# Kernel tuning notes

Hardware: AMD Instinct MI355X
Metric: run time of the kernel (lower is better)

Reference implementation:

```python
import jax, jax.numpy as jnp
import numpy as np

T, B, D_IN = 128, 256, 600   # timesteps, batch, encoded input dim
N_RIMS, K_ACT = 6, 4          # rims per layer, active rims (top-k)
D_HID = 600 // N_RIMS         # hidden dim per RIM = 100
D_K, D_V = 64, 400            # input-attention key/value proj dims (in_d_v = cell input dim)


def setup_inputs() -> dict:
    key = jax.random.key(0)
    ks = jax.random.split(key, 8)
    g = lambda k, shape, s: (jax.random.normal(k, shape, jnp.float32) * s)
    return {
        "x": jax.random.normal(ks[0], (T, B, D_IN), jnp.float32),
        # input attention: per-RIM query proj, shared key/value proj over encoded input
        "Wq": g(ks[1], (N_RIMS, D_HID, D_K), 0.05),
        "Wk": g(ks[2], (D_IN, D_K), 0.05),
        "Wv": g(ks[3], (D_IN, D_V), 0.05),
        # block-diagonal (per-RIM) GRU params
        "W_ih": g(ks[4], (N_RIMS, D_V, 3 * D_HID), 0.05),
        "W_hh": g(ks[5], (N_RIMS, D_HID, 3 * D_HID), 0.05),
        "b_ih": jnp.zeros((N_RIMS, 3 * D_HID), jnp.float32),
        "b_hh": jnp.zeros((N_RIMS, 3 * D_HID), jnp.float32),
    }


def reference(x, Wq, Wk, Wv, W_ih, W_hh, b_ih, b_hh):
    scale = 1.0 / jnp.sqrt(jnp.float32(D_K))

    def step(h, xt):
        # --- input attention over [real input, null row] (num_modules_read_input = 2) ---
        kx = xt @ Wk                                   # [B, D_K] key for real input (null key = 0)
        vx = xt @ Wv                                   # [B, D_V] value for real input (null value = 0)
        q = jnp.einsum('bnh,nhk->bnk', h, Wq)          # [B, N, D_K] per-RIM queries
        s_in = jnp.einsum('bnk,bk->bn', q, kx) * scale # score vs real input; null score = 0
        probs = jax.nn.softmax(jnp.stack([s_in, jnp.zeros_like(s_in)], axis=-1), axis=-1)
        p_in = probs[..., 0]                           # [B, N] attention on real input
        attn_out = p_in[..., None] * vx[:, None, :]    # [B, N, D_V] (null value is zero)
        # --- active-RIM mask: top-k rims attending most to the real input ---
        _, idx = jax.lax.top_k(p_in, K_ACT)            # [B, K]
        mask = jnp.zeros_like(p_in).at[jnp.arange(B)[:, None], idx].set(1.0)[..., None]  # [B, N, 1]
        # --- block-diagonal GRU cell (blockified params: independent per RIM) ---
        gi = jnp.einsum('bnd,ndk->bnk', attn_out, W_ih) + b_ih
        gh = jnp.einsum('bnh,nhk->bnk', h, W_hh) + b_hh
        i_r, i_z, i_n = jnp.split(gi, 3, axis=-1)
        h_r, h_z, h_n = jnp.split(gh, 3, axis=-1)
        r = jax.nn.sigmoid(i_r + h_r)
        z = jax.nn.sigmoid(i_z + h_z)
        n = jnp.tanh(i_n + r * h_n)
        h_new = (1.0 - z) * n + z * h
        # inactive rims keep their old state; output is mask * hidden
        h_next = mask * h_new + (1.0 - mask) * h
        return h_next, mask * h_new                    # [B, N, D_HID]

    h0 = jnp.zeros((B, N_RIMS, D_HID), x.dtype)
    _, out = jax.lax.scan(step, h0, x)                 # out: [T, B, N_RIMS, D_HID]
    return out
```

## Files before the change

kernel.cpp:

```cpp
#include <hip/hip_runtime.h>
#include <cstddef>

#define TSTEPS 128
#define BATCH  256
#define DIN    600
#define NR     6
#define KACT   4
#define DH     100
#define DK     64
#define DV     400
#define G3     300
#define LD1    512
#define LDG    1920
#define KB     8

__global__ __launch_bounds__(256) void build_w1(const float* __restrict__ Wk,
                                                const float* __restrict__ Wv,
                                                float* __restrict__ W1) {
  int idx = blockIdx.x * 256 + threadIdx.x;
  if (idx >= DIN * LD1) return;
  int d = idx >> 9, c = idx & (LD1 - 1);
  float v = 0.f;
  if (c < DK)            v = Wk[d * DK + c];
  else if (c < DK + DV)  v = Wv[d * DV + (c - DK)];
  W1[idx] = v;
}

__global__ __launch_bounds__(256) void build_wt(const float* __restrict__ Wih,
                                                float* __restrict__ WT) {
  int idx = blockIdx.x * 256 + threadIdx.x;
  if (idx >= DV * LDG) return;
  int v = idx / LDG, c = idx - v * LDG;
  float w = 0.f;
  if (c < NR * G3) { int n = c / G3, j = c - n * G3; w = Wih[(n * DV + v) * G3 + j]; }
  WT[idx] = w;
}

__global__ __launch_bounds__(256) void sgemm_k(const float* __restrict__ A, int lda,
                                               const float* __restrict__ B, int ldb,
                                               float* __restrict__ C, int ldc, int K) {
  __shared__ float As[2][KB][132];
  __shared__ float Bs[2][KB][192];
  const int tid = threadIdx.x;
  const int tx = tid & 15, ty = tid >> 4;
  const size_t m0 = (size_t)blockIdx.y * 128, n0 = (size_t)blockIdx.x * 128;
  const int arow = tid >> 1, akq = (tid & 1) * 4;
  const int brow = tid >> 5, bcol = (tid & 31) * 4;
  const int bphys = bcol + ((bcol >> 3) << 2);
  const float* Ap = A + (m0 + arow) * (size_t)lda + akq;
  const float* Bp = B + (size_t)brow * ldb + n0 + bcol;

  float acc[8][8];
#pragma unroll
  for (int i = 0; i < 8; ++i)
#pragma unroll
    for (int j = 0; j < 8; ++j) acc[i][j] = 0.f;

  const int NT = K / KB;
  float4 av = *(const float4*)(Ap);
  float4 bv = *(const float4*)(Bp);
  As[0][akq + 0][arow] = av.x;
  As[0][akq + 1][arow] = av.y;
  As[0][akq + 2][arow] = av.z;
  As[0][akq + 3][arow] = av.w;
  *(float4*)&Bs[0][brow][bphys] = bv;
  __syncthreads();

  int cur = 0;
  for (int it = 0; it < NT; ++it) {
    if (it + 1 < NT) {
      av = *(const float4*)(Ap + (it + 1) * KB);
      bv = *(const float4*)(Bp + (size_t)(it + 1) * KB * ldb);
    }
#pragma unroll
    for (int k = 0; k < KB; ++k) {
      float a[8], b[8];
      *(float4*)&a[0] = *(const float4*)&As[cur][k][ty * 8];
      *(float4*)&a[4] = *(const float4*)&As[cur][k][ty * 8 + 4];
      *(float4*)&b[0] = *(const float4*)&Bs[cur][k][tx * 12];
      *(float4*)&b[4] = *(const float4*)&Bs[cur][k][tx * 12 + 4];
#pragma unroll
      for (int i = 0; i < 8; ++i)
#pragma unroll
        for (int j = 0; j < 8; ++j) acc[i][j] += a[i] * b[j];
    }
    if (it + 1 < NT) {
      const int nxt = cur ^ 1;
      As[nxt][akq + 0][arow] = av.x;
      As[nxt][akq + 1][arow] = av.y;
      As[nxt][akq + 2][arow] = av.z;
      As[nxt][akq + 3][arow] = av.w;
      *(float4*)&Bs[nxt][brow][bphys] = bv;
      __syncthreads();
      cur = nxt;
    }
  }

  float* Cp = C + (m0 + (size_t)ty * 8) * ldc + n0 + tx * 8;
#pragma unroll
  for (int i = 0; i < 8; ++i) {
    float4 v0 = make_float4(acc[i][0], acc[i][1], acc[i][2], acc[i][3]);
    float4 v1 = make_float4(acc[i][4], acc[i][5], acc[i][6], acc[i][7]);
    *(float4*)(Cp + (size_t)i * ldc)     = v0;
    *(float4*)(Cp + (size_t)i * ldc + 4) = v1;
  }
}

__global__ __launch_bounds__(512) void rim_scan(
    const float* __restrict__ PRE1, const float* __restrict__ GX,
    const float* __restrict__ Wq,   const float* __restrict__ Whh,
    const float* __restrict__ bih,  const float* __restrict__ bhh,
    float* __restrict__ out, float* __restrict__ hstate,
    unsigned long long* __restrict__ pbuf,
    int t0, int tc, int first) {
  __shared__ __align__(16) float wbuf[G3 * DH];
  __shared__ __align__(16) float wqbuf[DK * DH];
  __shared__ __align__(16) float hbuf[8 * DH];
  __shared__ float pl[8][NR];

  const int tid = threadIdx.x;
  const int g = blockIdx.x & 31;
  const int n = blockIdx.x >> 5;

  {
    const float* wsrc = Whh + (size_t)n * (DH * G3);
    for (int i = tid; i < DH * G3; i += 512) {
      int hh = i / G3, c = i - hh * G3;
      wbuf[c * DH + hh] = wsrc[i];
    }
    const float* qsrc = Wq + (size_t)n * (DH * DK);
    for (int i = tid; i < DH * DK; i += 512) {
      int hh = i >> 6, k = i & 63;
      wqbuf[k * DH + hh] = qsrc[i];
    }
    if (first) {
      for (int i = tid; i < 8 * DH; i += 512) hbuf[i] = 0.f;
    } else {
      for (int i = tid; i < 8 * DH; i += 512) {
        int b = i / DH, hh = i - b * DH;
        hbuf[b * DH + hh] = hstate[((size_t)(g * 8 + b) * NR + n) * DH + hh];
      }
    }
  }
  __syncthreads();

  const bool isQ = tid >= 256;
  const int ho = tid & 127;
  const bool act_t = (!isQ) && (ho < DH);
  const int half = (tid >> 7) & 1;
  const int bbase = half * 4;
  const int kq = tid & 63;
  const int bp2 = (tid >> 6) & 3;

  float bi0 = 0.f, bi1 = 0.f, bi2 = 0.f, bh0 = 0.f, bh1 = 0.f, bh2 = 0.f;
  if (act_t) {
    const float* bi = bih + (size_t)n * G3 + ho;
    const float* bh = bhh + (size_t)n * G3 + ho;
    bi0 = bi[0]; bi1 = bi[DH]; bi2 = bi[2 * DH];
    bh0 = bh[0]; bh1 = bh[DH]; bh2 = bh[2 * DH];
  }

  const float4* wr = (const float4*)&wbuf[ho * DH];
  const float4* wz = (const float4*)&wbuf[(ho + 100) * DH];
  const float4* wn = (const float4*)&wbuf[(ho + 200) * DH];
  const float4* wq4 = (const float4*)&wqbuf[kq * DH];
  const float4* h40 = (const float4*)&hbuf[(bbase + 0) * DH];
  const float4* h41 = (const float4*)&hbuf[(bbase + 1) * DH];
  const float4* h42 = (const float4*)&hbuf[(bbase + 2) * DH];
  const float4* h43 = (const float4*)&hbuf[(bbase + 3) * DH];
  const float4* hqA = (const float4*)&hbuf[bp2 * DH];
  const float4* hqB = (const float4*)&hbuf[(bp2 + 4) * DH];

  for (int tl = 0; tl < tc; ++tl) {
    const int t = t0 + tl;
    const int par = t & 1;

    float gx[4][3];
    float acc[4][3];

    if (isQ) {
      float kx0 = PRE1[((size_t)tl * BATCH + g * 8 + bp2) * LD1 + kq];
      float kx1 = PRE1[((size_t)tl * BATCH + g * 8 + bp2 + 4) * LD1 + kq];
      float a0 = 0.f, a1 = 0.f;
#pragma unroll 5
      for (int q4 = 0; q4 < 25; ++q4) {
        float4 w = wq4[q4];
        float4 v0 = hqA[q4];
        float4 v1 = hqB[q4];
        a0 += v0.x * w.x; a0 += v0.y * w.y; a0 += v0.z * w.z; a0 += v0.w * w.w;
        a1 += v1.x * w.x; a1 += v1.y * w.y; a1 += v1.z * w.z; a1 += v1.w * w.w;
      }
      float s0 = a0 * kx0, s1 = a1 * kx1;
#pragma unroll
      for (int off = 1; off < 64; off <<= 1) {
        s0 += __shfl_xor(s0, off);
        s1 += __shfl_xor(s1, off);
      }
      if (kq == 0) {
        float sa = s0 * 0.125f;
        float ma = sa > 0.f ? sa : 0.f;
        float pa = expf(sa - ma) / (expf(sa - ma) + expf(-ma));
        float sb = s1 * 0.125f;
        float mb = sb > 0.f ? sb : 0.f;
        float pb = expf(sb - mb) / (expf(sb - mb) + expf(-mb));
        unsigned long long tag = ((unsigned long long)(unsigned)(t + 1)) << 32;
        __hip_atomic_store(&pbuf[(((size_t)par * 32 + g) * NR + n) * 8 + bp2],
                           tag | __float_as_uint(pa),
                           __ATOMIC_RELAXED, __HIP_MEMORY_SCOPE_AGENT);
        __hip_atomic_store(&pbuf[(((size_t)par * 32 + g) * NR + n) * 8 + bp2 + 4],
                           tag | __float_as_uint(pb),
                           __ATOMIC_RELAXED, __HIP_MEMORY_SCOPE_AGENT);
      }
    } else if (act_t) {
#pragma unroll
      for (int b = 0; b < 4; ++b) {
        const float* gr = GX + ((size_t)tl * BATCH + g * 8 + bbase + b) * LDG + n * G3;
        gx[b][0] = gr[ho]; gx[b][1] = gr[ho + DH]; gx[b][2] = gr[ho + 2 * DH];
      }
#pragma unroll
      for (int b = 0; b < 4; ++b) { acc[b][0] = 0.f; acc[b][1] = 0.f; acc[b][2] = 0.f; }
#pragma unroll 5
      for (int q4 = 0; q4 < 25; ++q4) {
        float4 w0 = wr[q4], w1 = wz[q4], w2 = wn[q4];
        float4 v0 = h40[q4], v1 = h41[q4], v2 = h42[q4], v3 = h43[q4];
        acc[0][0] += v0.x*w0.x; acc[0][0] += v0.y*w0.y; acc[0][0] += v0.z*w0.z; acc[0][0] += v0.w*w0.w;
        acc[0][1] += v0.x*w1.x; acc[0][1] += v0.y*w1.y; acc[0][1] += v0.z*w1.z; acc[0][1] += v0.w*w1.w;
        acc[0][2] += v0.x*w2.x; acc[0][2] += v0.y*w2.y; acc[0][2] += v0.z*w2.z; acc[0][2] += v0.w*w2.w;
        acc[1][0] += v1.x*w0.x; acc[1][0] += v1.y*w0.y; acc[1][0] += v1.z*w0.z; acc[1][0] += v1.w*w0.w;
        acc[1][1] += v1.x*w1.x; acc[1][1] += v1.y*w1.y; acc[1][1] += v1.z*w1.z; acc[1][1] += v1.w*w1.w;
        acc[1][2] += v1.x*w2.x; acc[1][2] += v1.y*w2.y; acc[1][2] += v1.z*w2.z; acc[1][2] += v1.w*w2.w;
        acc[2][0] += v2.x*w0.x; acc[2][0] += v2.y*w0.y; acc[2][0] += v2.z*w0.z; acc[2][0] += v2.w*w0.w;
        acc[2][1] += v2.x*w1.x; acc[2][1] += v2.y*w1.y; acc[2][1] += v2.z*w1.z; acc[2][1] += v2.w*w1.w;
        acc[2][2] += v2.x*w2.x; acc[2][2] += v2.y*w2.y; acc[2][2] += v2.z*w2.z; acc[2][2] += v2.w*w2.w;
        acc[3][0] += v3.x*w0.x; acc[3][0] += v3.y*w0.y; acc[3][0] += v3.z*w0.z; acc[3][0] += v3.w*w0.w;
        acc[3][1] += v3.x*w1.x; acc[3][1] += v3.y*w1.y; acc[3][1] += v3.z*w1.z; acc[3][1] += v3.w*w1.w;
        acc[3][2] += v3.x*w2.x; acc[3][2] += v3.y*w2.y; acc[3][2] += v3.z*w2.z; acc[3][2] += v3.w*w2.w;
      }
    }

    if (tid < 48) {
      int b = tid & 7, r = tid >> 3;
      const unsigned want = (unsigned)(t + 1);
      unsigned long long v;
      for (;;) {
        v = __hip_atomic_load(&pbuf[(((size_t)par * 32 + g) * NR + r) * 8 + b],
                              __ATOMIC_RELAXED, __HIP_MEMORY_SCOPE_AGENT);
        if ((unsigned)(v >> 32) == want) break;
        __builtin_amdgcn_s_sleep(1);
      }
      pl[b][r] = __uint_as_float((unsigned)v);
    }
    __syncthreads();

    if (act_t) {
#pragma unroll
      for (int b = 0; b < 4; ++b) {
        const int bb = bbase + b;
        float p = pl[bb][n];
        int c = 0;
#pragma unroll
        for (int r = 0; r < NR; ++r) {
          float q = pl[bb][r];
          if (q > p || (q == p && r < n)) ++c;
        }
        float m = (c < KACT) ? 1.f : 0.f;
        float grv = acc[b][0] + bh0;
        float gzv = acc[b][1] + bh1;
        float gnv = acc[b][2] + bh2;
        float ir  = p * gx[b][0] + bi0;
        float iz  = p * gx[b][1] + bi1;
        float inn = p * gx[b][2] + bi2;
        float rr = 1.f / (1.f + expf(-(ir + grv)));
        float zz = 1.f / (1.f + expf(-(iz + gzv)));
        float nn = tanhf(inn + rr * gnv);
        float hprev = hbuf[bb * DH + ho];
        float hnew = (1.f - zz) * nn + zz * hprev;
        out[(((size_t)t * BATCH + g * 8 + bb) * NR + n) * DH + ho] = m * hnew;
        hbuf[bb * DH + ho] = (m > 0.f) ? hnew : hprev;
      }
    }
    __syncthreads();
  }

  for (int i = tid; i < 8 * DH; i += 512) {
    int b = i / DH, hh = i - b * DH;
    hstate[((size_t)(g * 8 + b) * NR + n) * DH + hh] = hbuf[b * DH + hh];
  }
}

extern "C" void kernel_launch(void* const* d_in, const int* in_sizes, int n_in,
                              void* d_out, int out_size, void* d_ws, size_t ws_size,
                              hipStream_t stream) {
  const float* x   = (const float*)d_in[0];
  const float* Wq  = (const float*)d_in[1];
  const float* Wk  = (const float*)d_in[2];
  const float* Wv  = (const float*)d_in[3];
  const float* Wih = (const float*)d_in[4];
  const float* Whh = (const float*)d_in[5];
  const float* bih = (const float*)d_in[6];
  const float* bhh = (const float*)d_in[7];
  float* out = (float*)d_out;
  char* ws = (char*)d_ws;

  const size_t W1_BYTES   = (size_t)DIN * LD1 * 4;
  const size_t WT_BYTES   = (size_t)DV * LDG * 4;
  const size_t H_BYTES    = (size_t)BATCH * 600 * 4;
  const size_t PBUF_BYTES = 2 * 32 * NR * 8 * 8;
  const size_t FIXED = W1_BYTES + WT_BYTES + H_BYTES + PBUF_BYTES;
  const size_t PER_STEP = (size_t)BATCH * (LD1 + LDG) * 4;

  float* W1     = (float*)ws;
  float* WT     = (float*)(ws + W1_BYTES);
  float* hstate = (float*)(ws + W1_BYTES + WT_BYTES);
  unsigned long long* pbuf =
      (unsigned long long*)(ws + W1_BYTES + WT_BYTES + H_BYTES);

  long long avail = (long long)ws_size - (long long)FIXED;
  int TC = 1;
  if (avail > 0) {
    long long t = avail / (long long)PER_STEP;
    TC = (int)(t < 1 ? 1 : (t > TSTEPS ? TSTEPS : t));
  }
  float* PRE1 = (float*)(ws + FIXED);
  float* GXb  = (float*)(ws + FIXED + (size_t)TC * BATCH * LD1 * 4);

  build_w1<<<(DIN * LD1) / 256, 256, 0, stream>>>(Wk, Wv, W1);
  build_wt<<<(DV * LDG) / 256, 256, 0, stream>>>(Wih, WT);

  for (int t0 = 0; t0 < TSTEPS; ) {
    int tc = TSTEPS - t0 < TC ? TSTEPS - t0 : TC;
    dim3 g1(LD1 / 128, tc * 2);
    sgemm_k<<<g1, 256, 0, stream>>>(x + (size_t)t0 * BATCH * DIN, DIN, W1, LD1, PRE1, LD1, DIN);
    dim3 g2(LDG / 128, tc * 2);
    sgemm_k<<<g2, 256, 0, stream>>>(PRE1 + DK, LD1, WT, LDG, GXb, LDG, DV);
    rim_scan<<<32 * NR, 512, 0, stream>>>(PRE1, GXb, Wq, Whh, bih, bhh, out, hstate,
                                          pbuf, t0, tc, t0 == 0 ? 1 : 0);
    t0 += tc;
  }
}
```

Before: 1.905 ms.

## Repack W_hh into paired-column shared layout with two outputs per thread

Each GH thread now handles two adjacent hidden columns instead of one, which halves the active threads per half-batch from 100 to 50 lanes. W_hh is repacked in shared memory as float4 tiles interleaving two rows and two columns, so consecutive lanes read consecutive float4s with fewer bank conflicts. Loads of GX, stores to out and hbuf become float2 vectors. The aim is better LDS access efficiency and more register reuse of h values. The cost is fewer active lanes doing more serial work each, which may lengthen the critical path of every timestep.

```diff
diff --git a/kernel.cpp b/kernel.cpp
--- a/kernel.cpp
+++ b/kernel.cpp
@@ -113,7 +113,7 @@
     float* __restrict__ out, float* __restrict__ hstate,
     unsigned long long* __restrict__ pbuf,
     int t0, int tc, int first) {
-  __shared__ __align__(16) float wbuf[G3 * DH];
+  __shared__ __align__(16) float wpbuf[50 * 3 * 50 * 4];
   __shared__ __align__(16) float wqbuf[DK * DH];
   __shared__ __align__(16) float hbuf[8 * DH];
   __shared__ float pl[8][NR];
@@ -124,9 +124,18 @@
 
   {
     const float* wsrc = Whh + (size_t)n * (DH * G3);
-    for (int i = tid; i < DH * G3; i += 512) {
-      int hh = i / G3, c = i - hh * G3;
-      wbuf[c * DH + hh] = wsrc[i];
+    for (int i = tid; i < 50 * 3 * 50; i += 512) {
+      int ph = i / 150;
+      int r  = i - ph * 150;
+      int gg = r / 50;
+      int cp = r - gg * 50;
+      const float* base = wsrc + (2 * ph) * G3 + gg * 100 + 2 * cp;
+      float4 q;
+      q.x = base[0];
+      q.y = base[1];
+      q.z = base[G3];
+      q.w = base[G3 + 1];
+      *(float4*)&wpbuf[i * 4] = q;
     }
     const float* qsrc = Wq + (size_t)n * (DH * DK);
     for (int i = tid; i < DH * DK; i += 512) {
@@ -145,29 +154,33 @@
   __syncthreads();
 
   const bool isQ = tid >= 256;
-  const int ho = tid & 127;
-  const bool act_t = (!isQ) && (ho < DH);
-  const int half = (tid >> 7) & 1;
-  const int bbase = half * 4;
+  const int wv = tid >> 6, lane = tid & 63;
+  const bool ghA = (wv < 2) && (lane < 50);
+  const int bh = wv & 1;
+  const int cp = lane;
+  const int bbase = bh * 4;
   const int kq = tid & 63;
   const int bp2 = (tid >> 6) & 3;
 
-  float bi0 = 0.f, bi1 = 0.f, bi2 = 0.f, bh0 = 0.f, bh1 = 0.f, bh2 = 0.f;
-  if (act_t) {
-    const float* bi = bih + (size_t)n * G3 + ho;
-    const float* bh = bhh + (size_t)n * G3 + ho;
-    bi0 = bi[0]; bi1 = bi[DH]; bi2 = bi[2 * DH];
-    bh0 = bh[0]; bh1 = bh[DH]; bh2 = bh[2 * DH];
-  }
-
-  const float4* wr = (const float4*)&wbuf[ho * DH];
-  const float4* wz = (const float4*)&wbuf[(ho + 100) * DH];
-  const float4* wn = (const float4*)&wbuf[(ho + 200) * DH];
+  float bi_[3][2], bh_[3][2];
+  if (ghA) {
+#pragma unroll
+    for (int gg = 0; gg < 3; ++gg)
+#pragma unroll
+      for (int c = 0; c < 2; ++c) {
+        bi_[gg][c] = bih[(size_t)n * G3 + gg * 100 + 2 * cp + c];
+        bh_[gg][c] = bhh[(size_t)n * G3 + gg * 100 + 2 * cp + c];
+      }
+  }
+
+  const float4* wp = (const float4*)wpbuf;
   const float4* wq4 = (const float4*)&wqbuf[kq * DH];
-  const float4* h40 = (const float4*)&hbuf[(bbase + 0) * DH];
-  const float4* h41 = (const float4*)&hbuf[(bbase + 1) * DH];
-  const float4* h42 = (const float4*)&hbuf[(bbase + 2) * DH];
-  const float4* h43 = (const float4*)&hbuf[(bbase + 3) * DH];
+  const float4* hq4[4] = {
+    (const float4*)&hbuf[(bbase + 0) * DH],
+    (const float4*)&hbuf[(bbase + 1) * DH],
+    (const float4*)&hbuf[(bbase + 2) * DH],
+    (const float4*)&hbuf[(bbase + 3) * DH]
+  };
   const float4* hqA = (const float4*)&hbuf[bp2 * DH];
   const float4* hqB = (const float4*)&hbuf[(bp2 + 4) * DH];
 
@@ -175,8 +188,8 @@
     const int t = t0 + tl;
     const int par = t & 1;
 
-    float gx[4][3];
-    float acc[4][3];
+    float gx[4][3][2];
+    float acc[4][3][2];
 
     if (isQ) {
       float kx0 = PRE1[((size_t)tl * BATCH + g * 8 + bp2) * LD1 + kq];
@@ -211,30 +224,38 @@
                            tag | __float_as_uint(pb),
                            __ATOMIC_RELAXED, __HIP_MEMORY_SCOPE_AGENT);
       }
-    } else if (act_t) {
+    } else if (ghA) {
 #pragma unroll
       for (int b = 0; b < 4; ++b) {
         const float* gr = GX + ((size_t)tl * BATCH + g * 8 + bbase + b) * LDG + n * G3;
-        gx[b][0] = gr[ho]; gx[b][1] = gr[ho + DH]; gx[b][2] = gr[ho + 2 * DH];
-      }
-#pragma unroll
-      for (int b = 0; b < 4; ++b) { acc[b][0] = 0.f; acc[b][1] = 0.f; acc[b][2] = 0.f; }
+#pragma unroll
+        for (int gg = 0; gg < 3; ++gg) {
+          float2 v = *(const float2*)(gr + gg * 100 + 2 * cp);
+          gx[b][gg][0] = v.x; gx[b][gg][1] = v.y;
+        }
+      }
+#pragma unroll
+      for (int b = 0; b < 4; ++b)
+#pragma unroll
+        for (int gg = 0; gg < 3; ++gg) { acc[b][gg][0] = 0.f; acc[b][gg][1] = 0.f; }
 #pragma unroll 5
-      for (int q4 = 0; q4 < 25; ++q4) {
-        float4 w0 = wr[q4], w1 = wz[q4], w2 = wn[q4];
-        float4 v0 = h40[q4], v1 = h41[q4], v2 = h42[q4], v3 = h43[q4];
-        acc[0][0] += v0.x*w0.x; acc[0][0] += v0.y*w0.y; acc[0][0] += v0.z*w0.z; acc[0][0] += v0.w*w0.w;
-        acc[0][1] += v0.x*w1.x; acc[0][1] += v0.y*w1.y; acc[0][1] += v0.z*w1.z; acc[0][1] += v0.w*w1.w;
-        acc[0][2] += v0.x*w2.x; acc[0][2] += v0.y*w2.y; acc[0][2] += v0.z*w2.z; acc[0][2] += v0.w*w2.w;
-        acc[1][0] += v1.x*w0.x; acc[1][0] += v1.y*w0.y; acc[1][0] += v1.z*w0.z; acc[1][0] += v1.w*w0.w;
-        acc[1][1] += v1.x*w1.x; acc[1][1] += v1.y*w1.y; acc[1][1] += v1.z*w1.z; acc[1][1] += v1.w*w1.w;
-        acc[1][2] += v1.x*w2.x; acc[1][2] += v1.y*w2.y; acc[1][2] += v1.z*w2.z; acc[1][2] += v1.w*w2.w;
-        acc[2][0] += v2.x*w0.x; acc[2][0] += v2.y*w0.y; acc[2][0] += v2.z*w0.z; acc[2][0] += v2.w*w0.w;
-        acc[2][1] += v2.x*w1.x; acc[2][1] += v2.y*w1.y; acc[2][1] += v2.z*w1.z; acc[2][1] += v2.w*w1.w;
-        acc[2][2] += v2.x*w2.x; acc[2][2] += v2.y*w2.y; acc[2][2] += v2.z*w2.z; acc[2][2] += v2.w*w2.w;
-        acc[3][0] += v3.x*w0.x; acc[3][0] += v3.y*w0.y; acc[3][0] += v3.z*w0.z; acc[3][0] += v3.w*w0.w;
-        acc[3][1] += v3.x*w1.x; acc[3][1] += v3.y*w1.y; acc[3][1] += v3.z*w1.z; acc[3][1] += v3.w*w1.w;
-        acc[3][2] += v3.x*w2.x; acc[3][2] += v3.y*w2.y; acc[3][2] += v3.z*w2.z; acc[3][2] += v3.w*w2.w;
+      for (int pp = 0; pp < 25; ++pp) {
+        float4 wA0 = wp[(6 * pp + 0) * 50 + cp];
+        float4 wA1 = wp[(6 * pp + 1) * 50 + cp];
+        float4 wA2 = wp[(6 * pp + 2) * 50 + cp];
+        float4 wB0 = wp[(6 * pp + 3) * 50 + cp];
+        float4 wB1 = wp[(6 * pp + 4) * 50 + cp];
+        float4 wB2 = wp[(6 * pp + 5) * 50 + cp];
+#pragma unroll
+        for (int b = 0; b < 4; ++b) {
+          float4 h = hq4[b][pp];
+          acc[b][0][0] += h.x*wA0.x; acc[b][0][0] += h.y*wA0.z; acc[b][0][0] += h.z*wB0.x; acc[b][0][0] += h.w*wB0.z;
+          acc[b][0][1] += h.x*wA0.y; acc[b][0][1] += h.y*wA0.w; acc[b][0][1] += h.z*wB0.y; acc[b][0][1] += h.w*wB0.w;
+          acc[b][1][0] += h.x*wA1.x; acc[b][1][0] += h.y*wA1.z; acc[b][1][0] += h.z*wB1.x; acc[b][1][0] += h.w*wB1.z;
+          acc[b][1][1] += h.x*wA1.y; acc[b][1][1] += h.y*wA1.w; acc[b][1][1] += h.z*wB1.y; acc[b][1][1] += h.w*wB1.w;
+          acc[b][2][0] += h.x*wA2.x; acc[b][2][0] += h.y*wA2.z; acc[b][2][0] += h.z*wB2.x; acc[b][2][0] += h.w*wB2.z;
+          acc[b][2][1] += h.x*wA2.y; acc[b][2][1] += h.y*wA2.w; acc[b][2][1] += h.z*wB2.y; acc[b][2][1] += h.w*wB2.w;
+        }
       }
     }
 
@@ -252,7 +273,7 @@
     }
     __syncthreads();
 
-    if (act_t) {
+    if (ghA) {
 #pragma unroll
       for (int b = 0; b < 4; ++b) {
         const int bb = bbase + b;
@@ -264,19 +285,27 @@
           if (q > p || (q == p && r < n)) ++c;
         }
         float m = (c < KACT) ? 1.f : 0.f;
-        float grv = acc[b][0] + bh0;
-        float gzv = acc[b][1] + bh1;
-        float gnv = acc[b][2] + bh2;
-        float ir  = p * gx[b][0] + bi0;
-        float iz  = p * gx[b][1] + bi1;
-        float inn = p * gx[b][2] + bi2;
-        float rr = 1.f / (1.f + expf(-(ir + grv)));
-        float zz = 1.f / (1.f + expf(-(iz + gzv)));
-        float nn = tanhf(inn + rr * gnv);
-        float hprev = hbuf[bb * DH + ho];
-        float hnew = (1.f - zz) * nn + zz * hprev;
-        out[(((size_t)t * BATCH + g * 8 + bb) * NR + n) * DH + ho] = m * hnew;
-        hbuf[bb * DH + ho] = (m > 0.f) ? hnew : hprev;
+        float hn2[2];
+#pragma unroll
+        for (int cc = 0; cc < 2; ++cc) {
+          float grv = acc[b][0][cc] + bh_[0][cc];
+          float gzv = acc[b][1][cc] + bh_[1][cc];
+          float gnv = acc[b][2][cc] + bh_[2][cc];
+          float ir  = p * gx[b][0][cc] + bi_[0][cc];
+          float iz  = p * gx[b][1][cc] + bi_[1][cc];
+          float inn = p * gx[b][2][cc] + bi_[2][cc];
+          float rr = 1.f / (1.f + expf(-(ir + grv)));
+          float zz = 1.f / (1.f + expf(-(iz + gzv)));
+          float nn = tanhf(inn + rr * gnv);
+          float hprev = hbuf[bb * DH + 2 * cp + cc];
+          float hnew = (1.f - zz) * nn + zz * hprev;
+          hn2[cc] = hnew;
+        }
+        float2 ov = make_float2(m * hn2[0], m * hn2[1]);
+        *(float2*)&out[(((size_t)t * BATCH + g * 8 + bb) * NR + n) * DH + 2 * cp] = ov;
+        if (m > 0.f) {
+          *(float2*)&hbuf[bb * DH + 2 * cp] = make_float2(hn2[0], hn2[1]);
+        }
       }
     }
     __syncthreads();
```

Result: slower. 2.183 ms (+14.6%).
